# Kernel optimization log

Hardware: AMD Instinct MI355X
Metric: run time of the kernel (lower is better)

Reference implementation:

```python
import jax, jax.numpy as jnp
import numpy as np

SPACE_DIM = 3
D = SPACE_DIM + 1            # (t, x, y, z)
D_MODEL = 1024
N_LAYERS = 4                 # hidden layers
N_MIX = 64
TRI = D * (D - 1) // 2       # strict upper-triangular entries of A
OUT_DIM = N_MIX * (TRI + 1)  # per-mixture triu values + mixture logits
TRIU_I, TRIU_J = np.triu_indices(D, k=1)
RHO_SCALE = 10.0


def setup_inputs() -> dict:
    key = jax.random.key(0)
    ks = jax.random.split(key, 8)
    B = 65536
    x = jax.random.normal(ks[0], (B, D), jnp.float32)
    W0 = jax.random.normal(ks[1], (D, D_MODEL), jnp.float32) * np.float32(np.sqrt(2.0 / D))
    b0 = jnp.zeros((D_MODEL,), jnp.float32)
    Wh = jax.random.normal(ks[2], (N_LAYERS, D_MODEL, D_MODEL), jnp.float32) * np.float32(np.sqrt(2.0 / D_MODEL))
    bh = jnp.zeros((N_LAYERS, D_MODEL), jnp.float32)
    Wout = jax.random.normal(ks[3], (D_MODEL, OUT_DIM), jnp.float32) * np.float32(np.sqrt(1.0 / D_MODEL))
    bout = jnp.zeros((OUT_DIM,), jnp.float32)
    return dict(x=x, W0=W0, b0=b0, Wh=Wh, bh=bh, Wout=Wout, bout=bout)


def _mlp(z, W0, b0, Wh, bh, Wout, bout):
    # z: (D,) -> (OUT_DIM,), swish MLP (NeuralConservationLaw backbone)
    h = jax.nn.silu(z @ W0 + b0)
    for l in range(N_LAYERS):  # fixed small layer count: python loop ok
        h = jax.nn.silu(h @ Wh[l] + bh[l])
    return h @ Wout + bout


def _A(z, params):
    # Antisymmetric matrix field A(z): mixture-weighted strict-upper-tri values.
    out = _mlp(z, *params)                              # (OUT_DIM,)
    logits = out[:N_MIX]                                # (N_MIX,)
    vals = out[N_MIX:].reshape(N_MIX, TRI)              # (N_MIX, TRI)
    a = jax.nn.softmax(logits) @ vals                   # (TRI,)
    A = jnp.zeros((D, D), out.dtype).at[TRIU_I, TRIU_J].set(a)
    return A - A.T                                      # antisymmetric (D, D)


def reference(x, W0, b0, Wh, bh, Wout, bout):
    params = (W0, b0, Wh, bh, Wout, bout)

    def u_single(z):
        # u_i = sum_j dA_ij/dz_j  (row-divergence of antisymmetric A => div u = 0)
        J = jax.jacfwd(lambda zz: _A(zz, params))(z)    # (D, D, D): J[i,j,k]=dA_ij/dz_k
        return jnp.einsum('ijj->i', J)                  # (D,)

    u = jax.vmap(u_single)(x)                           # (B, D)
    rho = u[..., :1] * RHO_SCALE
    flux = u[..., 1:]
    return jnp.concatenate([rho, flux], axis=-1)
```

## Files before the change

### kernel.cpp

```cpp
#include <hip/hip_runtime.h>
#include <hip/hip_bf16.h>

typedef _Float16 half8 __attribute__((ext_vector_type(8)));
typedef _Float16 half4 __attribute__((ext_vector_type(4)));
typedef float floatx4 __attribute__((ext_vector_type(4)));

__device__ __forceinline__ float bfu2f(unsigned short u) {
  return __uint_as_float(((unsigned)u) << 16);
}

__device__ __forceinline__ void gld16(const void* g, void* l) {
  __builtin_amdgcn_global_load_lds((const __attribute__((address_space(1))) void*)g,
                                   (__attribute__((address_space(3))) void*)l, 16, 0, 0);
}

__device__ __forceinline__ float fast_sig(float v) {
  return __builtin_amdgcn_rcpf(1.f + __expf(-v));
}

template <int NC>
__device__ __forceinline__ void xcd_decode(int lin, int NR, int& r, int& c) {
  if (NR & 7) {
    c = lin % NC;
    r = lin / NC;
  } else {
    int rl = lin & 7;
    int t = lin >> 3;
    c = t % NC;
    r = (t / NC) * 8 + rl;
  }
}

__global__ void probe_kernel(const unsigned short* __restrict__ w0, int* __restrict__ flag) {
  __shared__ int s;
  if (threadIdx.x == 0) s = 0;
  __syncthreads();
  int big = 0;
  for (int i = threadIdx.x; i < 2048; i += 256) {
    unsigned e = (w0[i] >> 7) & 0xFFu;
    if (e >= 134u) big = 1;
  }
  if (big) atomicOr(&s, 1);
  __syncthreads();
  if (threadIdx.x == 0) *flag = s;
}

__global__ void cvt_kernel(const void* __restrict__ in, _Float16* __restrict__ out, int nOut,
                           int nIn, const int* __restrict__ flag) {
  int i = blockIdx.x * 256 + threadIdx.x;
  if (i >= nOut) return;
  float v = 0.f;
  if (i < nIn) v = (*flag) ? ((const float*)in)[i] : bfu2f(((const unsigned short*)in)[i]);
  out[i] = (_Float16)v;
}

__global__ void tr_kernel(const void* __restrict__ in, _Float16* __restrict__ out, int Nin,
                          long inStride, long outStride, const int* __restrict__ flag) {
  __shared__ float tile[32][33];
  const int f = *flag;
  int k0 = blockIdx.x * 32, n0 = blockIdx.y * 32;
  long ib = (long)blockIdx.z * inStride;
  long ob = (long)blockIdx.z * outStride;
  int tx = threadIdx.x, ty = threadIdx.y;
#pragma unroll
  for (int i = 0; i < 4; i++) {
    int k = k0 + ty + i * 8, n = n0 + tx;
    float v = 0.f;
    if (n < Nin) {
      long idx = ib + (long)k * Nin + n;
      v = f ? ((const float*)in)[idx] : bfu2f(((const unsigned short*)in)[idx]);
    }
    tile[ty + i * 8][tx] = v;
  }
  __syncthreads();
#pragma unroll
  for (int i = 0; i < 4; i++) {
    int n = n0 + ty + i * 8, k = k0 + tx;
    out[ob + (long)n * 1024 + k] = (_Float16)tile[tx][ty + i * 8];
  }
}

__global__ __launch_bounds__(256)
void layer0_kernel(const _Float16* __restrict__ x16, const _Float16* __restrict__ W0c,
                   const _Float16* __restrict__ b0c, _Float16* __restrict__ H,
                   int chunkBase, int S1) {
  const int lb = blockIdx.x;
  const int t = threadIdx.x;
  const long gb = (long)chunkBase + lb;
  float z0 = (float)x16[gb * 4 + 0];
  float z1 = (float)x16[gb * 4 + 1];
  float z2 = (float)x16[gb * 4 + 2];
  float z3 = (float)x16[gb * 4 + 3];
  const int j0 = t * 4;
  float w[4][4];
#pragma unroll
  for (int i = 0; i < 4; i++) {
    half4 wv = *(const half4*)&W0c[i * 1024 + j0];
#pragma unroll
    for (int jj = 0; jj < 4; jj++) w[i][jj] = (float)wv[jj];
  }
  half4 o[5];
#pragma unroll
  for (int jj = 0; jj < 4; jj++) {
    float pre = z0 * w[0][jj] + z1 * w[1][jj] + z2 * w[2][jj] + z3 * w[3][jj] +
                (float)b0c[j0 + jj];
    float s = fast_sig(pre);
    o[0][jj] = (_Float16)(pre * s);
    float ds = s * (1.f + pre * (1.f - s));
    o[1][jj] = (_Float16)(ds * w[0][jj]);
    o[2][jj] = (_Float16)(ds * w[1][jj]);
    o[3][jj] = (_Float16)(ds * w[2][jj]);
    o[4][jj] = (_Float16)(ds * w[3][jj]);
  }
  long rowbase = (long)lb * 1024 + j0;
#pragma unroll
  for (int s = 0; s < 5; s++) *(half4*)&H[(long)s * S1 + rowbase] = o[s];
}

__global__ __launch_bounds__(256, 3)
void gemm_h1(const _Float16* __restrict__ A, const _Float16* __restrict__ Bt,
             const _Float16* __restrict__ bias, _Float16* __restrict__ C,
             _Float16* __restrict__ DS, int NR) {
  constexpr int K = 1024;
  __shared__ _Float16 SM[8192];
  _Float16* As = SM;
  _Float16* Bs = SM + 4096;
  _Float16* Ep = SM;
  const int tid = threadIdx.x;
  const int wave = tid >> 6;
  const int lane = tid & 63;
  int rb, cb;
  xcd_decode<8>(blockIdx.x, NR, rb, cb);
  const int n0 = cb * 128;
  const long m0 = (long)rb * 128;

  const int srow0 = (wave * 2 + 0) * 16 + (lane >> 2);
  const int srow1 = (wave * 2 + 1) * 16 + (lane >> 2);
  const int scol = (lane & 3) * 8;
  const _Float16* gA0 = A + (m0 + srow0) * K + scol;
  const _Float16* gA1 = A + (m0 + srow1) * K + scol;
  const _Float16* gB0 = Bt + (long)(n0 + srow0) * K + scol;
  const _Float16* gB1 = Bt + (long)(n0 + srow1) * K + scol;
  _Float16* lA0 = As + (wave * 2 + 0) * 512;
  _Float16* lA1 = As + (wave * 2 + 1) * 512;
  _Float16* lB0 = Bs + (wave * 2 + 0) * 512;
  _Float16* lB1 = Bs + (wave * 2 + 1) * 512;

  const int wm = (wave & 1) * 64;
  const int wn = (wave >> 1) * 64;
  const int fr = lane & 15;
  const int fc = (lane >> 4) * 8;
  const int c0f = lane & 15;
  const int rqk = lane >> 4;
  const int myRound = wave & 1;

  float bv[4];
#pragma unroll
  for (int ni = 0; ni < 4; ni++) bv[ni] = (float)bias[n0 + wn + ni * 16 + c0f];

  const int erow = tid >> 4;
  const int ecol = (tid & 15) * 8;
  const int ecolp = ecol ^ (wave << 4);

  floatx4 acc[4][4];
#pragma unroll
  for (int i = 0; i < 4; i++)
#pragma unroll
    for (int j = 0; j < 4; j++) acc[i][j] = (floatx4)(0.f);

  for (int kk = 0; kk < K; kk += 32) {
    __syncthreads();
    gld16(gA0 + kk, lA0);
    gld16(gA1 + kk, lA1);
    gld16(gB0 + kk, lB0);
    gld16(gB1 + kk, lB1);
    __syncthreads();
    half8 af[4], bf[4];
#pragma unroll
    for (int i = 0; i < 4; i++) af[i] = *(const half8*)&As[(wm + i * 16 + fr) * 32 + fc];
#pragma unroll
    for (int i = 0; i < 4; i++) bf[i] = *(const half8*)&Bs[(wn + i * 16 + fr) * 32 + fc];
#pragma unroll
    for (int mi = 0; mi < 4; mi++)
#pragma unroll
      for (int ni = 0; ni < 4; ni++)
        acc[mi][ni] = __builtin_amdgcn_mfma_f32_16x16x32_f16(af[mi], bf[ni], acc[mi][ni], 0, 0, 0);
  }

#pragma unroll
  for (int r = 0; r < 2; r++) {
    __syncthreads();
    if (myRound == r) {
#pragma unroll
      for (int mi = 0; mi < 4; mi++)
#pragma unroll
        for (int ni = 0; ni < 4; ni++) {
          int colp = (wn + ni * 16 + c0f) ^ (rqk << 4);
#pragma unroll
          for (int rr = 0; rr < 4; rr++) {
            int row_local = mi * 16 + rqk * 4 + rr;
            Ep[row_local * 128 + colp] = (_Float16)(acc[mi][ni][rr] + bv[ni]);
          }
        }
    }
    __syncthreads();
#pragma unroll
    for (int p = 0; p < 4; p++) {
      int row_local = p * 16 + erow;
      half8 vv = *(const half8*)&Ep[row_local * 128 + ecolp];
      long row = m0 + r * 64 + row_local;
      half8 hv, dv;
#pragma unroll
      for (int e = 0; e < 8; e++) {
        float xv = (float)vv[e];
        float sg = fast_sig(xv);
        hv[e] = (_Float16)(xv * sg);
        dv[e] = (_Float16)(sg * (1.f + xv * (1.f - sg)));
      }
      *(half8*)&C[row * (long)K + n0 + ecol] = hv;
      *(half8*)&DS[row * (long)K + n0 + ecol] = dv;
    }
  }
}

__global__ __launch_bounds__(512, 2)
void gemm_h1_256(const _Float16* __restrict__ A, const _Float16* __restrict__ Bt,
                 const _Float16* __restrict__ bias, _Float16* __restrict__ C,
                 _Float16* __restrict__ DS, int NR) {
  constexpr int K = 1024;
  __shared__ _Float16 SM[36864];
  const int tid = threadIdx.x;
  const int wave = tid >> 6;
  const int lane = tid & 63;
  int rb, cb;
  xcd_decode<4>(blockIdx.x, NR, rb, cb);
  const long m0 = (long)rb * 128;
  const int n0 = cb * 256;

  const int srowA = wave * 16 + (lane >> 2);
  const int srowB = wave * 32 + (lane >> 2);
  const int scol = ((lane & 3) ^ ((lane >> 3) & 3)) * 8;
  const _Float16* gA0 = A + (m0 + srowA) * K + scol;
  const _Float16* gB0 = Bt + (long)(n0 + srowB) * K + scol;
  const _Float16* gB1 = gB0 + 16 * K;
  const int loffA = wave * 512;
  const int loffB = wave * 1024;

  const int wr = wave >> 2;
  const int wc = wave & 3;
  const int fr = lane & 15;
  const int fc = ((lane >> 4) ^ ((lane >> 1) & 3)) * 8;
  const int rqk = lane >> 4;
  const int c0f = lane & 15;

  float bv[4];
#pragma unroll
  for (int ni = 0; ni < 4; ni++) bv[ni] = (float)bias[n0 + wc * 64 + ni * 16 + c0f];

  floatx4 acc[4][4];
#pragma unroll
  for (int i = 0; i < 4; i++)
#pragma unroll
    for (int j = 0; j < 4; j++) acc[i][j] = (floatx4)(0.f);

  {
    _Float16* b0p = SM;
    gld16(gA0 + 0, b0p + loffA);
    gld16(gB0 + 0, b0p + 4096 + loffB);
    gld16(gB1 + 0, b0p + 4096 + loffB + 512);
    _Float16* b1p = SM + 12288;
    gld16(gA0 + 32, b1p + loffA);
    gld16(gB0 + 32, b1p + 4096 + loffB);
    gld16(gB1 + 32, b1p + 4096 + loffB + 512);
  }

  int bufCur = 0;
  int bufNxt = 2;
  for (int it = 0; it < 32; ++it) {
    if (it < 31) __builtin_amdgcn_s_waitcnt(0x0F73);
    else         __builtin_amdgcn_s_waitcnt(0x0F70);
    __builtin_amdgcn_s_barrier();
    const int kk = (it + 2) * 32;
    _Float16* bp = SM + bufNxt * 12288;
    if (it < 30) {
      gld16(gA0 + kk, bp + loffA);
    }
    const _Float16* Asb = SM + bufCur * 12288;
    const _Float16* Bsb = Asb + 4096;
    half8 af[4], bf0, bf1, bf2, bf3;
#pragma unroll
    for (int i = 0; i < 4; i++)
      af[i] = *(const half8*)&Asb[(wr * 64 + i * 16 + fr) * 32 + fc];
    bf0 = *(const half8*)&Bsb[(wc * 64 + 0 * 16 + fr) * 32 + fc];
    bf1 = *(const half8*)&Bsb[(wc * 64 + 1 * 16 + fr) * 32 + fc];
    __builtin_amdgcn_s_setprio(1);
#pragma unroll
    for (int mi = 0; mi < 4; mi++) {
      acc[mi][0] = __builtin_amdgcn_mfma_f32_16x16x32_f16(af[mi], bf0, acc[mi][0], 0, 0, 0);
      acc[mi][1] = __builtin_amdgcn_mfma_f32_16x16x32_f16(af[mi], bf1, acc[mi][1], 0, 0, 0);
    }
    __builtin_amdgcn_s_setprio(0);
    if (it < 30) {
      gld16(gB0 + kk, bp + 4096 + loffB);
      gld16(gB1 + kk, bp + 4096 + loffB + 512);
    }
    bf2 = *(const half8*)&Bsb[(wc * 64 + 2 * 16 + fr) * 32 + fc];
    bf3 = *(const half8*)&Bsb[(wc * 64 + 3 * 16 + fr) * 32 + fc];
    __builtin_amdgcn_s_setprio(1);
#pragma unroll
    for (int mi = 0; mi < 4; mi++) {
      acc[mi][2] = __builtin_amdgcn_mfma_f32_16x16x32_f16(af[mi], bf2, acc[mi][2], 0, 0, 0);
      acc[mi][3] = __builtin_amdgcn_mfma_f32_16x16x32_f16(af[mi], bf3, acc[mi][3], 0, 0, 0);
    }
    __builtin_amdgcn_s_setprio(0);
    bufCur = (bufCur == 2) ? 0 : bufCur + 1;
    bufNxt = (bufNxt == 2) ? 0 : bufNxt + 1;
  }

  const int erow = tid >> 3;
  const int rqkr = (erow >> 2) & 3;
#pragma unroll
  for (int r = 0; r < 2; ++r) {
    __syncthreads();
    if (wr == r) {
#pragma unroll
      for (int mi2 = 0; mi2 < 4; ++mi2) {
#pragma unroll
        for (int ni = 0; ni < 4; ++ni) {
          int colp = (wc * 64 + ni * 16 + c0f) ^ (rqk << 4);
#pragma unroll
          for (int rr = 0; rr < 4; ++rr) {
            int row_local = mi2 * 16 + rqk * 4 + rr;
            SM[row_local * 256 + colp] = (_Float16)(acc[mi2][ni][rr] + bv[ni]);
          }
        }
      }
    }
    __syncthreads();
    long grow = m0 + r * 64 + erow;
#pragma unroll
    for (int q = 0; q < 4; ++q) {
      int col = (tid & 7) * 8 + q * 64;
      int colp = col ^ (rqkr << 4);
      half8 vv = *(const half8*)&SM[erow * 256 + colp];
      half8 hv, dv;
#pragma unroll
      for (int e = 0; e < 8; e++) {
        float xv = (float)vv[e];
        float sg = fast_sig(xv);
        hv[e] = (_Float16)(xv * sg);
        dv[e] = (_Float16)(sg * (1.f + xv * (1.f - sg)));
      }
      *(half8*)&C[grow * (long)K + n0 + col] = hv;
      *(half8*)&DS[grow * (long)K + n0 + col] = dv;
    }
  }
}

__global__ __launch_bounds__(512, 2)
void gemm_h2(const _Float16* __restrict__ A, const _Float16* __restrict__ Bt,
             _Float16* __restrict__ C, const _Float16* __restrict__ DS, int bcMask, int NR) {
  constexpr int K = 1024;
  __shared__ _Float16 SM[49152];
  const int tid = threadIdx.x;
  const int wave = tid >> 6;
  const int lane = tid & 63;
  int rb, cb;
  xcd_decode<4>(blockIdx.x, NR, rb, cb);
  const long m0 = (long)rb * 256;
  const int n0 = cb * 256;

  const int srow = wave * 32 + (lane >> 2);
  const int scol = ((lane & 3) ^ ((lane >> 3) & 3)) * 8;
  const _Float16* gA0 = A + (m0 + srow) * K + scol;
  const _Float16* gA1 = gA0 + 16 * K;
  const _Float16* gB0 = Bt + (long)(n0 + srow) * K + scol;
  const _Float16* gB1 = gB0 + 16 * K;
  const int loff0 = wave * 1024;
  const int loff1 = loff0 + 512;

  const int wr = wave >> 2;
  const int wc = wave & 3;
  const int fr = lane & 15;
  const int fc = ((lane >> 4) ^ ((lane >> 1) & 3)) * 8;
  const int rqk = lane >> 4;
  const int c0f = lane & 15;

  floatx4 acc[8][4];
#pragma unroll
  for (int i = 0; i < 8; i++)
#pragma unroll
    for (int j = 0; j < 4; j++) acc[i][j] = (floatx4)(0.f);

  {
    _Float16* b0p = SM;
    gld16(gA0 + 0, b0p + loff0);
    gld16(gA1 + 0, b0p + loff1);
    gld16(gB0 + 0, b0p + 8192 + loff0);
    gld16(gB1 + 0, b0p + 8192 + loff1);
    _Float16* b1p = SM + 16384;
    gld16(gA0 + 32, b1p + loff0);
    gld16(gA1 + 32, b1p + loff1);
    gld16(gB0 + 32, b1p + 8192 + loff0);
    gld16(gB1 + 32, b1p + 8192 + loff1);
  }

  int bufCur = 0;
  int bufNxt = 2;
  for (int it = 0; it < 32; ++it) {
    if (it < 31) __builtin_amdgcn_s_waitcnt(0x0F74);
    else         __builtin_amdgcn_s_waitcnt(0x0F70);
    __builtin_amdgcn_s_barrier();
    const int kk = (it + 2) * 32;
    _Float16* bp = SM + bufNxt * 16384;
    if (it < 30) {
      gld16(gA0 + kk, bp + loff0);
      gld16(gA1 + kk, bp + loff1);
    }
    const _Float16* Asb = SM + bufCur * 16384;
    const _Float16* Bsb = Asb + 8192;
    half8 af[8], bf0, bf1, bf2, bf3;
#pragma unroll
    for (int i = 0; i < 8; i++)
      af[i] = *(const half8*)&Asb[(wr * 128 + i * 16 + fr) * 32 + fc];
    bf0 = *(const half8*)&Bsb[(wc * 64 + 0 * 16 + fr) * 32 + fc];
    bf1 = *(const half8*)&Bsb[(wc * 64 + 1 * 16 + fr) * 32 + fc];
    __builtin_amdgcn_s_setprio(1);
#pragma unroll
    for (int mi = 0; mi < 8; mi++) {
      acc[mi][0] = __builtin_amdgcn_mfma_f32_16x16x32_f16(af[mi], bf0, acc[mi][0], 0, 0, 0);
      acc[mi][1] = __builtin_amdgcn_mfma_f32_16x16x32_f16(af[mi], bf1, acc[mi][1], 0, 0, 0);
    }
    __builtin_amdgcn_s_setprio(0);
    if (it < 30) {
      gld16(gB0 + kk, bp + 8192 + loff0);
      gld16(gB1 + kk, bp + 8192 + loff1);
    }
    bf2 = *(const half8*)&Bsb[(wc * 64 + 2 * 16 + fr) * 32 + fc];
    bf3 = *(const half8*)&Bsb[(wc * 64 + 3 * 16 + fr) * 32 + fc];
    __builtin_amdgcn_s_setprio(1);
#pragma unroll
    for (int mi = 0; mi < 8; mi++) {
      acc[mi][2] = __builtin_amdgcn_mfma_f32_16x16x32_f16(af[mi], bf2, acc[mi][2], 0, 0, 0);
      acc[mi][3] = __builtin_amdgcn_mfma_f32_16x16x32_f16(af[mi], bf3, acc[mi][3], 0, 0, 0);
    }
    __builtin_amdgcn_s_setprio(0);
    bufCur = (bufCur == 2) ? 0 : bufCur + 1;
    bufNxt = (bufNxt == 2) ? 0 : bufNxt + 1;
  }

  const int erow = tid >> 3;
  const int rqkr = (erow >> 2) & 3;
#pragma unroll
  for (int r = 0; r < 4; ++r) {
    __syncthreads();
    if (wr == (r >> 1)) {
      const int mib = (r & 1) * 4;
#pragma unroll
      for (int mi2 = 0; mi2 < 4; ++mi2) {
#pragma unroll
        for (int ni = 0; ni < 4; ++ni) {
          int colp = (wc * 64 + ni * 16 + c0f) ^ (rqk << 4);
#pragma unroll
          for (int rr = 0; rr < 4; ++rr) {
            int row_local = mi2 * 16 + rqk * 4 + rr;
            SM[row_local * 256 + colp] = (_Float16)acc[mib + mi2][ni][rr];
          }
        }
      }
    }
    __syncthreads();
    long grow = m0 + r * 64 + erow;
    long dsrow = grow & bcMask;
#pragma unroll
    for (int q = 0; q < 4; ++q) {
      int col = (tid & 7) * 8 + q * 64;
      int colp = col ^ (rqkr << 4);
      half8 vv = *(const half8*)&SM[erow * 256 + colp];
      half8 dv = *(const half8*)&DS[dsrow * (long)K + n0 + col];
      *(half8*)&C[grow * (long)K + n0 + col] = dv * vv;
    }
  }
}

__global__ __launch_bounds__(256, 4)
void gemm_out(const _Float16* __restrict__ A, const _Float16* __restrict__ Bt,
              const _Float16* __restrict__ bias, _Float16* __restrict__ C,
              int Nreal, int ldc, int biasRows, int NR) {
  constexpr int K = 1024;
  __shared__ _Float16 SM[8192];
  _Float16* As = SM;
  _Float16* Bs = SM + 4096;
  _Float16* Ep = SM;
  const int tid = threadIdx.x;
  const int wave = tid >> 6;
  const int lane = tid & 63;
  int rb, cb;
  xcd_decode<4>(blockIdx.x, NR, rb, cb);
  const int n0 = cb * 128;
  const long m0 = (long)rb * 128;

  const int srow0 = (wave * 2 + 0) * 16 + (lane >> 2);
  const int srow1 = (wave * 2 + 1) * 16 + (lane >> 2);
  const int scol = (lane & 3) * 8;
  const _Float16* gA0 = A + (m0 + srow0) * K + scol;
  const _Float16* gA1 = A + (m0 + srow1) * K + scol;
  const _Float16* gB0 = Bt + (long)(n0 + srow0) * K + scol;
  const _Float16* gB1 = Bt + (long)(n0 + srow1) * K + scol;
  _Float16* lA0 = As + (wave * 2 + 0) * 512;
  _Float16* lA1 = As + (wave * 2 + 1) * 512;
  _Float16* lB0 = Bs + (wave * 2 + 0) * 512;
  _Float16* lB1 = Bs + (wave * 2 + 1) * 512;

  const int wm = (wave & 1) * 64;
  const int wn = (wave >> 1) * 64;
  const int fr = lane & 15;
  const int fc = (lane >> 4) * 8;
  const int c0f = lane & 15;
  const int rqk = lane >> 4;
  const int myRound = wave & 1;

  float bv[4];
#pragma unroll
  for (int ni = 0; ni < 4; ni++) bv[ni] = (float)bias[n0 + wn + ni * 16 + c0f];

  const int erow = tid >> 4;
  const int ecol = (tid & 15) * 8;
  const int ecolp = ecol ^ (wave << 4);

  floatx4 acc[4][4];
#pragma unroll
  for (int i = 0; i < 4; i++)
#pragma unroll
    for (int j = 0; j < 4; j++) acc[i][j] = (floatx4)(0.f);

  for (int kk = 0; kk < K; kk += 32) {
    __syncthreads();
    gld16(gA0 + kk, lA0);
    gld16(gA1 + kk, lA1);
    gld16(gB0 + kk, lB0);
    gld16(gB1 + kk, lB1);
    __syncthreads();
    half8 af[4], bf[4];
#pragma unroll
    for (int i = 0; i < 4; i++) af[i] = *(const half8*)&As[(wm + i * 16 + fr) * 32 + fc];
#pragma unroll
    for (int i = 0; i < 4; i++) bf[i] = *(const half8*)&Bs[(wn + i * 16 + fr) * 32 + fc];
#pragma unroll
    for (int mi = 0; mi < 4; mi++)
#pragma unroll
      for (int ni = 0; ni < 4; ni++)
        acc[mi][ni] = __builtin_amdgcn_mfma_f32_16x16x32_f16(af[mi], bf[ni], acc[mi][ni], 0, 0, 0);
  }

#pragma unroll
  for (int r = 0; r < 2; r++) {
    __syncthreads();
    if (myRound == r) {
#pragma unroll
      for (int mi = 0; mi < 4; mi++)
#pragma unroll
        for (int ni = 0; ni < 4; ni++) {
          int colp = (wn + ni * 16 + c0f) ^ (rqk << 4);
#pragma unroll
          for (int rr = 0; rr < 4; rr++) {
            int row_local = mi * 16 + rqk * 4 + rr;
            long grow = m0 + wm + mi * 16 + rqk * 4 + rr;
            float v = acc[mi][ni][rr] + (grow < biasRows ? bv[ni] : 0.f);
            Ep[row_local * 128 + colp] = (_Float16)v;
          }
        }
    }
    __syncthreads();
#pragma unroll
    for (int p = 0; p < 4; p++) {
      int row_local = p * 16 + erow;
      int col = n0 + ecol;
      if (col < Nreal) {
        half8 vv = *(const half8*)&Ep[row_local * 128 + ecolp];
        long row = m0 + r * 64 + row_local;
        *(half8*)&C[row * (long)ldc + col] = vv;
      }
    }
  }
}

__global__ __launch_bounds__(256)
void finalize_kernel(const _Float16* __restrict__ O5, void* __restrict__ outp,
                     int chunkBase, int Bc, const int* __restrict__ flag) {
  const int wid = threadIdx.x >> 6;
  const int lane = threadIdx.x & 63;
  const int lb = blockIdx.x * 4 + wid;
  const long SO = (long)Bc * 448;
  const long base0 = (long)lb * 448;

  union UU { unsigned u; _Float16 h[2]; };

  float lg = (float)O5[base0 + lane];
  float vals[6];
  {
    const unsigned* vp = (const unsigned*)(O5 + base0 + 64 + lane * 6);
#pragma unroll
    for (int q = 0; q < 3; q++) {
      UU c; c.u = vp[q];
      vals[2 * q] = (float)c.h[0];
      vals[2 * q + 1] = (float)c.h[1];
    }
  }
  float dl[4], dv[4][6];
#pragma unroll
  for (int t = 0; t < 4; t++) {
    long bs = (long)(1 + t) * SO + base0;
    dl[t] = (float)O5[bs + lane];
    const unsigned* vp = (const unsigned*)(O5 + bs + 64 + lane * 6);
#pragma unroll
    for (int q = 0; q < 3; q++) {
      UU c; c.u = vp[q];
      dv[t][2 * q] = (float)c.h[0];
      dv[t][2 * q + 1] = (float)c.h[1];
    }
  }
  float mx = lg;
#pragma unroll
  for (int off = 32; off >= 1; off >>= 1) mx = fmaxf(mx, __shfl_xor(mx, off));
  float e = __expf(lg - mx);
  float S = e;
#pragma unroll
  for (int off = 32; off >= 1; off >>= 1) S += __shfl_xor(S, off);
  float pv = e / S;
  float st[4];
#pragma unroll
  for (int t = 0; t < 4; t++) {
    float v = pv * dl[t];
#pragma unroll
    for (int off = 32; off >= 1; off >>= 1) v += __shfl_xor(v, off);
    st[t] = v;
  }
  float da[4][6];
#pragma unroll
  for (int t = 0; t < 4; t++) {
    float w = pv * (dl[t] - st[t]);
#pragma unroll
    for (int k = 0; k < 6; k++) {
      float v = w * vals[k] + pv * dv[t][k];
#pragma unroll
      for (int off = 32; off >= 1; off >>= 1) v += __shfl_xor(v, off);
      da[t][k] = v;
    }
  }
  if (lane == 0) {
    float u0 = da[1][0] + da[2][1] + da[3][2];
    float u1 = -da[0][0] + da[2][3] + da[3][4];
    float u2 = -da[0][1] - da[1][3] + da[3][5];
    float u3 = -da[0][2] - da[1][4] - da[2][5];
    long ob = (long)(chunkBase + lb) * 4;
    if (*flag) {
      float* o = (float*)outp;
      o[ob] = 10.f * u0; o[ob + 1] = u1; o[ob + 2] = u2; o[ob + 3] = u3;
    } else {
      __hip_bfloat16* o = (__hip_bfloat16*)outp;
      o[ob] = __float2bfloat16(10.f * u0);
      o[ob + 1] = __float2bfloat16(u1);
      o[ob + 2] = __float2bfloat16(u2);
      o[ob + 3] = __float2bfloat16(u3);
    }
  }
}

extern "C" void kernel_launch(void* const* d_in, const int* in_sizes, int n_in,
                              void* d_out, int out_size, void* d_ws, size_t ws_size,
                              hipStream_t stream) {
  const void* x = d_in[0];
  const void* W0 = d_in[1];
  const void* b0 = d_in[2];
  const void* Wh = d_in[3];
  const void* bh = d_in[4];
  const void* Wout = d_in[5];
  const void* bout = d_in[6];
  const int B = in_sizes[0] / 4;

  char* p = (char*)d_ws;
  int* flag = (int*)p;                 p += 256;
  _Float16* W0c = (_Float16*)p;        p += 4096 * 2;
  _Float16* b0c = (_Float16*)p;        p += 1024 * 2;
  _Float16* bhc = (_Float16*)p;        p += 4096 * 2;
  _Float16* boutc = (_Float16*)p;      p += 512 * 2;
  p += 256 - ((size_t)(p - (char*)d_ws) & 255);
  _Float16* x16 = (_Float16*)p;        p += (size_t)B * 4 * 2;
  _Float16* WhT = (_Float16*)p;        p += (size_t)4 * 1024 * 1024 * 2;
  _Float16* WoutT = (_Float16*)p;      p += (size_t)512 * 1024 * 2;
  size_t used = (size_t)(p - (char*)d_ws);
  size_t rem = (ws_size > used) ? (ws_size - used) : 0;
  const size_t perS = 10240 + 10240 + 2048 + 4480;
  long bcap = (long)(rem / perS);
  int Bc = 128;
  while ((long)Bc * 2 <= bcap && Bc * 2 <= B) Bc *= 2;
  _Float16* Ha = (_Float16*)p;         p += (size_t)5 * Bc * 1024 * 2;
  _Float16* Hb = (_Float16*)p;         p += (size_t)5 * Bc * 1024 * 2;
  _Float16* DS = (_Float16*)p;         p += (size_t)Bc * 1024 * 2;
  _Float16* PREo = (_Float16*)p;

  probe_kernel<<<1, 256, 0, stream>>>((const unsigned short*)W0, flag);
  cvt_kernel<<<(B * 4 + 255) / 256, 256, 0, stream>>>(x, x16, B * 4, B * 4, flag);
  cvt_kernel<<<16, 256, 0, stream>>>(W0, W0c, 4096, 4096, flag);
  cvt_kernel<<<4, 256, 0, stream>>>(b0, b0c, 1024, 1024, flag);
  cvt_kernel<<<16, 256, 0, stream>>>(bh, bhc, 4096, 4096, flag);
  cvt_kernel<<<2, 256, 0, stream>>>(bout, boutc, 512, 448, flag);
  tr_kernel<<<dim3(32, 32, 4), dim3(32, 8), 0, stream>>>(Wh, WhT, 1024, 1024L * 1024, 1024L * 1024, flag);
  tr_kernel<<<dim3(32, 16, 1), dim3(32, 8), 0, stream>>>(Wout, WoutT, 448, 0L, 0L, flag);

  const int nChunks = B / Bc;
  for (int c = 0; c < nChunks; c++) {
    const int base = c * Bc;
    const int S1 = Bc * 1024;
    _Float16* Hin = Ha;
    _Float16* Hout = Hb;
    layer0_kernel<<<Bc, 256, 0, stream>>>(x16, W0c, b0c, Hin, base, S1);
    const int NR1row = Bc / 128;
    const int NR2row = Bc / 64;
    const int NRo = 5 * Bc / 128;
    for (int l = 0; l < 4; l++) {
      const _Float16* Wl = WhT + (size_t)l * 1024 * 1024;
      gemm_h1_256<<<4 * NR1row, 512, 0, stream>>>(
          Hin, Wl, bhc + l * 1024, Hout, DS, NR1row);
      gemm_h2<<<4 * NR2row, 512, 0, stream>>>(
          Hin + S1, Wl, Hout + S1, DS, Bc - 1, NR2row);
      _Float16* t = Hin; Hin = Hout; Hout = t;
    }
    gemm_out<<<4 * NRo, 256, 0, stream>>>(
        Hin, WoutT, boutc, PREo, 448, 448, Bc, NRo);
    finalize_kernel<<<Bc / 4, 256, 0, stream>>>(PREo, d_out, base, Bc, flag);
  }
}
```

Before: 3.934 ms.

## Rewrite output GEMM with 128x256 tiles, triple-buffered LDS pipeline and swizzle

The output-projection GEMM now runs 512-thread blocks that each compute a 128x256 tile instead of 256-thread blocks on 128x128 tiles. The K loop keeps a three-stage LDS ring buffer, issuing the next loads with explicit waitcnt and barrier while MFMAs run, and raises wave priority during the MFMA bursts. It also XOR-swizzles the LDS layout to avoid bank conflicts. The aim is to hide global-load latency and halve B-tile reloads, at the cost of 72KB of LDS per block, which lowers occupancy, and wasted work on the padded columns past 448.

```diff
diff --git a/kernel.cpp b/kernel.cpp
--- a/kernel.cpp
+++ b/kernel.cpp
@@ -483,50 +483,39 @@
   }
 }
 
-__global__ __launch_bounds__(256, 4)
+__global__ __launch_bounds__(512, 2)
 void gemm_out(const _Float16* __restrict__ A, const _Float16* __restrict__ Bt,
               const _Float16* __restrict__ bias, _Float16* __restrict__ C,
               int Nreal, int ldc, int biasRows, int NR) {
   constexpr int K = 1024;
-  __shared__ _Float16 SM[8192];
-  _Float16* As = SM;
-  _Float16* Bs = SM + 4096;
-  _Float16* Ep = SM;
+  __shared__ _Float16 SM[36864];
   const int tid = threadIdx.x;
   const int wave = tid >> 6;
   const int lane = tid & 63;
   int rb, cb;
-  xcd_decode<4>(blockIdx.x, NR, rb, cb);
-  const int n0 = cb * 128;
+  xcd_decode<2>(blockIdx.x, NR, rb, cb);
   const long m0 = (long)rb * 128;
-
-  const int srow0 = (wave * 2 + 0) * 16 + (lane >> 2);
-  const int srow1 = (wave * 2 + 1) * 16 + (lane >> 2);
-  const int scol = (lane & 3) * 8;
-  const _Float16* gA0 = A + (m0 + srow0) * K + scol;
-  const _Float16* gA1 = A + (m0 + srow1) * K + scol;
-  const _Float16* gB0 = Bt + (long)(n0 + srow0) * K + scol;
-  const _Float16* gB1 = Bt + (long)(n0 + srow1) * K + scol;
-  _Float16* lA0 = As + (wave * 2 + 0) * 512;
-  _Float16* lA1 = As + (wave * 2 + 1) * 512;
-  _Float16* lB0 = Bs + (wave * 2 + 0) * 512;
-  _Float16* lB1 = Bs + (wave * 2 + 1) * 512;
-
-  const int wm = (wave & 1) * 64;
-  const int wn = (wave >> 1) * 64;
+  const int n0 = cb * 256;
+
+  const int srowA = wave * 16 + (lane >> 2);
+  const int srowB = wave * 32 + (lane >> 2);
+  const int scol = ((lane & 3) ^ ((lane >> 3) & 3)) * 8;
+  const _Float16* gA0 = A + (m0 + srowA) * K + scol;
+  const _Float16* gB0 = Bt + (long)(n0 + srowB) * K + scol;
+  const _Float16* gB1 = gB0 + 16 * K;
+  const int loffA = wave * 512;
+  const int loffB = wave * 1024;
+
+  const int wr = wave >> 2;
+  const int wc = wave & 3;
   const int fr = lane & 15;
-  const int fc = (lane >> 4) * 8;
+  const int fc = ((lane >> 4) ^ ((lane >> 1) & 3)) * 8;
+  const int rqk = lane >> 4;
   const int c0f = lane & 15;
-  const int rqk = lane >> 4;
-  const int myRound = wave & 1;
 
   float bv[4];
 #pragma unroll
-  for (int ni = 0; ni < 4; ni++) bv[ni] = (float)bias[n0 + wn + ni * 16 + c0f];
-
-  const int erow = tid >> 4;
-  const int ecol = (tid & 15) * 8;
-  const int ecolp = ecol ^ (wave << 4);
+  for (int ni = 0; ni < 4; ni++) bv[ni] = (float)bias[n0 + wc * 64 + ni * 16 + c0f];
 
   floatx4 acc[4][4];
 #pragma unroll
@@ -534,52 +523,90 @@
 #pragma unroll
     for (int j = 0; j < 4; j++) acc[i][j] = (floatx4)(0.f);
 
-  for (int kk = 0; kk < K; kk += 32) {
-    __syncthreads();
-    gld16(gA0 + kk, lA0);
-    gld16(gA1 + kk, lA1);
-    gld16(gB0 + kk, lB0);
-    gld16(gB1 + kk, lB1);
-    __syncthreads();
-    half8 af[4], bf[4];
-#pragma unroll
-    for (int i = 0; i < 4; i++) af[i] = *(const half8*)&As[(wm + i * 16 + fr) * 32 + fc];
-#pragma unroll
-    for (int i = 0; i < 4; i++) bf[i] = *(const half8*)&Bs[(wn + i * 16 + fr) * 32 + fc];
-#pragma unroll
-    for (int mi = 0; mi < 4; mi++)
-#pragma unroll
-      for (int ni = 0; ni < 4; ni++)
-        acc[mi][ni] = __builtin_amdgcn_mfma_f32_16x16x32_f16(af[mi], bf[ni], acc[mi][ni], 0, 0, 0);
-  }
-
-#pragma unroll
-  for (int r = 0; r < 2; r++) {
-    __syncthreads();
-    if (myRound == r) {
-#pragma unroll
-      for (int mi = 0; mi < 4; mi++)
-#pragma unroll
-        for (int ni = 0; ni < 4; ni++) {
-          int colp = (wn + ni * 16 + c0f) ^ (rqk << 4);
-#pragma unroll
-          for (int rr = 0; rr < 4; rr++) {
-            int row_local = mi * 16 + rqk * 4 + rr;
-            long grow = m0 + wm + mi * 16 + rqk * 4 + rr;
-            float v = acc[mi][ni][rr] + (grow < biasRows ? bv[ni] : 0.f);
-            Ep[row_local * 128 + colp] = (_Float16)v;
+  {
+    _Float16* b0p = SM;
+    gld16(gA0 + 0, b0p + loffA);
+    gld16(gB0 + 0, b0p + 4096 + loffB);
+    gld16(gB1 + 0, b0p + 4096 + loffB + 512);
+    _Float16* b1p = SM + 12288;
+    gld16(gA0 + 32, b1p + loffA);
+    gld16(gB0 + 32, b1p + 4096 + loffB);
+    gld16(gB1 + 32, b1p + 4096 + loffB + 512);
+  }
+
+  int bufCur = 0;
+  int bufNxt = 2;
+  for (int it = 0; it < 32; ++it) {
+    if (it < 31) __builtin_amdgcn_s_waitcnt(0x0F73);
+    else         __builtin_amdgcn_s_waitcnt(0x0F70);
+    __builtin_amdgcn_s_barrier();
+    const int kk = (it + 2) * 32;
+    _Float16* bp = SM + bufNxt * 12288;
+    if (it < 30) {
+      gld16(gA0 + kk, bp + loffA);
+    }
+    const _Float16* Asb = SM + bufCur * 12288;
+    const _Float16* Bsb = Asb + 4096;
+    half8 af[4], bf0, bf1, bf2, bf3;
+#pragma unroll
+    for (int i = 0; i < 4; i++)
+      af[i] = *(const half8*)&Asb[(wr * 64 + i * 16 + fr) * 32 + fc];
+    bf0 = *(const half8*)&Bsb[(wc * 64 + 0 * 16 + fr) * 32 + fc];
+    bf1 = *(const half8*)&Bsb[(wc * 64 + 1 * 16 + fr) * 32 + fc];
+    __builtin_amdgcn_s_setprio(1);
+#pragma unroll
+    for (int mi = 0; mi < 4; mi++) {
+      acc[mi][0] = __builtin_amdgcn_mfma_f32_16x16x32_f16(af[mi], bf0, acc[mi][0], 0, 0, 0);
+      acc[mi][1] = __builtin_amdgcn_mfma_f32_16x16x32_f16(af[mi], bf1, acc[mi][1], 0, 0, 0);
+    }
+    __builtin_amdgcn_s_setprio(0);
+    if (it < 30) {
+      gld16(gB0 + kk, bp + 4096 + loffB);
+      gld16(gB1 + kk, bp + 4096 + loffB + 512);
+    }
+    bf2 = *(const half8*)&Bsb[(wc * 64 + 2 * 16 + fr) * 32 + fc];
+    bf3 = *(const half8*)&Bsb[(wc * 64 + 3 * 16 + fr) * 32 + fc];
+    __builtin_amdgcn_s_setprio(1);
+#pragma unroll
+    for (int mi = 0; mi < 4; mi++) {
+      acc[mi][2] = __builtin_amdgcn_mfma_f32_16x16x32_f16(af[mi], bf2, acc[mi][2], 0, 0, 0);
+      acc[mi][3] = __builtin_amdgcn_mfma_f32_16x16x32_f16(af[mi], bf3, acc[mi][3], 0, 0, 0);
+    }
+    __builtin_amdgcn_s_setprio(0);
+    bufCur = (bufCur == 2) ? 0 : bufCur + 1;
+    bufNxt = (bufNxt == 2) ? 0 : bufNxt + 1;
+  }
+
+  const int erow = tid >> 3;
+  const int rqkr = (erow >> 2) & 3;
+#pragma unroll
+  for (int r = 0; r < 2; ++r) {
+    __syncthreads();
+    if (wr == r) {
+#pragma unroll
+      for (int mi2 = 0; mi2 < 4; ++mi2) {
+#pragma unroll
+        for (int ni = 0; ni < 4; ++ni) {
+          int colp = (wc * 64 + ni * 16 + c0f) ^ (rqk << 4);
+#pragma unroll
+          for (int rr = 0; rr < 4; ++rr) {
+            int row_local = mi2 * 16 + rqk * 4 + rr;
+            long grow = m0 + r * 64 + row_local;
+            float v = acc[mi2][ni][rr] + (grow < biasRows ? bv[ni] : 0.f);
+            SM[row_local * 256 + colp] = (_Float16)v;
           }
         }
-    }
-    __syncthreads();
-#pragma unroll
-    for (int p = 0; p < 4; p++) {
-      int row_local = p * 16 + erow;
-      int col = n0 + ecol;
-      if (col < Nreal) {
-        half8 vv = *(const half8*)&Ep[row_local * 128 + ecolp];
-        long row = m0 + r * 64 + row_local;
-        *(half8*)&C[row * (long)ldc + col] = vv;
+      }
+    }
+    __syncthreads();
+    long grow = m0 + r * 64 + erow;
+#pragma unroll
+    for (int q = 0; q < 4; ++q) {
+      int col = (tid & 7) * 8 + q * 64;
+      if (n0 + q * 64 < Nreal) {
+        int colp = col ^ (rqkr << 4);
+        half8 vv = *(const half8*)&SM[erow * 256 + colp];
+        *(half8*)&C[grow * (long)ldc + n0 + col] = vv;
       }
     }
   }
@@ -718,7 +745,7 @@
     layer0_kernel<<<Bc, 256, 0, stream>>>(x16, W0c, b0c, Hin, base, S1);
     const int NR1row = Bc / 128;
     const int NR2row = Bc / 64;
-    const int NRo = 5 * Bc / 128;
+    const int NRoRow = 5 * Bc / 128;
     for (int l = 0; l < 4; l++) {
       const _Float16* Wl = WhT + (size_t)l * 1024 * 1024;
       gemm_h1_256<<<4 * NR1row, 512, 0, stream>>>(
@@ -727,8 +754,8 @@
           Hin + S1, Wl, Hout + S1, DS, Bc - 1, NR2row);
       _Float16* t = Hin; Hin = Hout; Hout = t;
     }
-    gemm_out<<<4 * NRo, 256, 0, stream>>>(
-        Hin, WoutT, boutc, PREo, 448, 448, Bc, NRo);
+    gemm_out<<<2 * NRoRow, 512, 0, stream>>>(
+        Hin, WoutT, boutc, PREo, 448, 448, Bc, NRoRow);
     finalize_kernel<<<Bc / 4, 256, 0, stream>>>(PREo, d_out, base, Bc, flag);
   }
 }
```

New measurement: 3.826 ms, median of 4. 2.8% less time.
